# Optimization experiments

Hardware: AMD Instinct MI355X
Metric: run time of the kernel (lower is better)

The kernel has to match this reference:

```python
import jax, jax.numpy as jnp
import numpy as np

V, E, H, L = 100000, 128, 512, 9
B, T = 64, 512


def setup_inputs() -> dict:
    key = jax.random.key(0)
    ks = jax.random.split(key, 8)
    text = jax.random.randint(ks[0], (B, T), 0, V, dtype=jnp.int32)
    labels = jax.random.randint(ks[1], (B, T), 0, L, dtype=jnp.int32)
    embed = jax.random.normal(ks[2], (V, E), jnp.float32) * 0.02
    Wx = jax.random.normal(ks[3], (E, 4 * H), jnp.float32) * (1.0 / np.sqrt(E))
    Wh = jax.random.normal(ks[4], (H, 4 * H), jnp.float32) * (1.0 / np.sqrt(H))
    # Keras LSTM default: zero bias with unit forget-gate bias (gate order i,f,c,o)
    b = jnp.zeros((4 * H,), jnp.float32).at[H:2 * H].set(1.0)
    Wd = jax.random.normal(ks[5], (H, L), jnp.float32) * (1.0 / np.sqrt(H))
    bd = jnp.zeros((L,), jnp.float32)
    trans = jax.random.uniform(ks[6], (L, L), jnp.float32)
    return dict(text=text, labels=labels, embed=embed, Wx=Wx, Wh=Wh, b=b,
                Wd=Wd, bd=bd, trans=trans)


def _lstm(x, Wx, Wh, b):
    # x: [B,T,E] -> h: [B,T,H]; Keras gate order i,f,c,o
    Bx, Tx, _ = x.shape
    Hh = Wh.shape[0]
    xg = jnp.einsum('bte,eg->btg', x, Wx) + b  # precompute input projections [B,T,4H]

    def step(carry, g_t):
        h, c = carry
        g = g_t + h @ Wh
        i, f, cg, o = jnp.split(g, 4, axis=-1)
        c = jax.nn.sigmoid(f) * c + jax.nn.sigmoid(i) * jnp.tanh(cg)
        h = jax.nn.sigmoid(o) * jnp.tanh(c)
        return (h, c), h

    init = (jnp.zeros((Bx, Hh), x.dtype), jnp.zeros((Bx, Hh), x.dtype))
    _, hs = jax.lax.scan(step, init, jnp.moveaxis(xg, 1, 0))
    return jnp.moveaxis(hs, 0, 1)


def _crf_log_likelihood(logits, labels, lens, trans):
    # tfa.text.crf_log_likelihood: score(seq) - log_norm (forward algorithm)
    Bl, Tl, Ll = logits.shape
    t_idx = jnp.arange(Tl)
    mask = t_idx[None, :] < lens[:, None]  # [B,T]
    unary = jnp.take_along_axis(logits, labels[..., None], axis=2)[..., 0]
    unary = jnp.where(mask, unary, 0.0).sum(-1)
    binary = trans[labels[:, :-1], labels[:, 1:]]
    bmask = t_idx[1:][None, :] < lens[:, None]  # transition t->t+1 counts iff t+1 < len
    binary = jnp.where(bmask, binary, 0.0).sum(-1)
    score = unary + binary

    def step(alpha, xs):
        lg, t = xs  # lg: [B,L]
        new = jax.scipy.special.logsumexp(alpha[:, :, None] + trans[None], axis=1) + lg
        alpha = jnp.where((t < lens)[:, None], new, alpha)
        return alpha, None

    alpha0 = logits[:, 0]
    xs = (jnp.moveaxis(logits[:, 1:], 1, 0), jnp.arange(1, Tl))
    alpha, _ = jax.lax.scan(step, alpha0, xs)
    log_norm = jax.scipy.special.logsumexp(alpha, axis=-1)
    return score - log_norm


def reference(text, labels, embed, Wx, Wh, b, Wd, bd, trans):
    lens = jnp.sum((text != 0).astype(jnp.int32), axis=-1)
    x = embed[text]                      # [B,T,E] (dropout inactive at inference)
    h = _lstm(x, Wx, Wh, b)              # [B,T,H]
    logits = h @ Wd + bd                 # [B,T,L]
    ll = _crf_log_likelihood(logits, labels, lens, trans)  # [B]
    return logits, lens, ll
```

## Files before the change

### kernel.cpp

```cpp
#include <hip/hip_runtime.h>
#include <hip/hip_bf16.h>

#define V_SZ 100000
#define E_SZ 128
#define H_SZ 512
#define L_SZ 9
#define B_SZ 64
#define T_SZ 512
#define G4   (4*H_SZ)

#define LOGITS_N (B_SZ*T_SZ*L_SZ)
#define HS_BYTES ((size_t)B_SZ*T_SZ*H_SZ*2)
#define SENT32 0x7FC07FC0u
#define SENT64 0x7FC07FC07FC07FC0ull

typedef short bf16x8 __attribute__((ext_vector_type(8)));
typedef float f32x4  __attribute__((ext_vector_type(4)));

static __device__ __forceinline__ unsigned short f2bf(float x){
  unsigned int u = __builtin_bit_cast(unsigned int, x);
  unsigned int r = (u + 0x7fffu + ((u >> 16) & 1u)) >> 16;
  return (unsigned short)r;
}
static __device__ __forceinline__ float bf2f(unsigned short b){
  unsigned int u = ((unsigned int)b) << 16;
  return __builtin_bit_cast(float, u);
}
static __device__ __forceinline__ float sig_f(float x){
  return 1.f / (1.f + __expf(-x));
}
static __device__ __forceinline__ float tanh_f(float x){
  float a = fabsf(x);
  float e = __expf(-2.f * a);
  float t = (1.f - e) / (1.f + e);
  return copysignf(t, x);
}

__global__ void k_reset(unsigned long long* __restrict__ hs64){
  const long n = HS_BYTES / 8;
  for (long i = (long)blockIdx.x*256 + threadIdx.x; i < n; i += (long)gridDim.x*256)
    __hip_atomic_store(&hs64[i], SENT64, __ATOMIC_RELAXED, __HIP_MEMORY_SCOPE_AGENT);
}

__global__ void k_lens(const int* __restrict__ text, float* __restrict__ out_lens){
  int b = blockIdx.x;
  int c = 0;
  for (int t = threadIdx.x; t < T_SZ; t += 256)
    c += (text[b*T_SZ + t] != 0);
  for (int off = 32; off; off >>= 1) c += __shfl_down(c, off, 64);
  __shared__ int sred[4];
  int w = threadIdx.x >> 6;
  if ((threadIdx.x & 63) == 0) sred[w] = c;
  __syncthreads();
  if (threadIdx.x == 0)
    out_lens[b] = (float)(sred[0] + sred[1] + sred[2] + sred[3]);
}

__global__ __launch_bounds__(256, 1)
void k_lstm(const int* __restrict__ text, const float* __restrict__ embed,
            const float* __restrict__ Wx, const float* __restrict__ Wh,
            const float* __restrict__ bias, unsigned short* __restrict__ hs)
{
  const int g    = blockIdx.x & 7;
  const int j    = blockIdx.x >> 3;
  const int n0   = j * 16;
  const int tid  = threadIdx.x;
  const int w    = tid >> 6;
  const int lane = tid & 63;
  const int q    = lane >> 4;
  const int l16  = lane & 15;
  const int gate = l16 & 3;
  const int cq   = l16 >> 2;

  __shared__ unsigned short h_lds[2][16*512];
  __shared__ unsigned short x_lds[2][16*128];

  for (int i = tid; i < 2*16*512; i += 256) ((unsigned short*)h_lds)[i] = 0;
  for (int i = tid; i < 2*16*128; i += 256) ((unsigned short*)x_lds)[i] = 0;

  const int hcol = n0 + w*4 + cq;
  const int gcol = gate*H_SZ + hcol;
  bf16x8 Whf[16];
#pragma unroll
  for (int kk = 0; kk < 16; ++kk){
    bf16x8 v;
#pragma unroll
    for (int jj = 0; jj < 8; ++jj)
      v[jj] = (short)f2bf(Wh[(long)(kk*32 + q*8 + jj)*G4 + gcol]);
    Whf[kk] = v;
  }
  bf16x8 Wxf[4];
#pragma unroll
  for (int kk = 0; kk < 4; ++kk){
    bf16x8 v;
#pragma unroll
    for (int jj = 0; jj < 8; ++jj)
      v[jj] = (short)f2bf(Wx[(long)(kk*32 + q*8 + jj)*G4 + gcol]);
    Wxf[kk] = v;
  }
  const float biasv = bias[gcol];

  float cs[4] = {0.f, 0.f, 0.f, 0.f};
  const bool isPub = (gate == 0) && ((cq & 1) == 0) && (q < 2);

  unsigned short* ppub[4];
#pragma unroll
  for (int rg = 0; rg < 4; ++rg)
    ppub[rg] = hs + ((long)(g*8 + q*4 + rg)*T_SZ)*H_SZ + n0 + w*4 + cq;

  __syncthreads();

  for (int t = 0; t < T_SZ; ++t){
    const int par = t & 1;

    {
      int xr = tid >> 5;
      int c4 = (tid & 31) * 4;
      int idx = text[(g*8 + xr)*T_SZ + t];
      const float4 xv = *(const float4*)(embed + (long)idx*E_SZ + c4);
      int cb = c4 * 2;
      unsigned short* pp = (unsigned short*)((char*)x_lds[par] + xr*256 + (cb ^ (xr << 4)));
      pp[0] = f2bf(xv.x); pp[1] = f2bf(xv.y); pp[2] = f2bf(xv.z); pp[3] = f2bf(xv.w);
    }

    if (t > 0){
      unsigned long long v[4];
      int it = 0; bool ok;
      do {
        ok = true;
#pragma unroll
        for (int c = 0; c < 4; ++c){
          int chunk = tid + 256*c;
          int hr    = chunk >> 7;
          int k4    = chunk & 127;
          v[c] = __hip_atomic_load(
              (const unsigned long long*)(hs + ((long)(g*8 + hr)*T_SZ + (t-1))*H_SZ + k4*4),
              __ATOMIC_RELAXED, __HIP_MEMORY_SCOPE_AGENT);
        }
#pragma unroll
        for (int c = 0; c < 4; ++c){
          unsigned int lo = (unsigned int)v[c], hi = (unsigned int)(v[c] >> 32);
          ok = ok && (lo != SENT32) && (hi != SENT32);
        }
      } while (!ok && ++it < (1 << 20));
#pragma unroll
      for (int c = 0; c < 4; ++c){
        int chunk = tid + 256*c;
        int hr    = chunk >> 7;
        int k4    = chunk & 127;
        *(unsigned long long*)((char*)h_lds[par] + hr*1024 + ((k4*8) ^ (hr << 4))) = v[c];
      }
    }
    __syncthreads();

    f32x4 acc0 = {biasv, biasv, biasv, biasv};
    f32x4 acc1 = {0.f, 0.f, 0.f, 0.f};
#pragma unroll
    for (int kk = 0; kk < 4; ++kk){
      bf16x8 a = *(const bf16x8*)((const char*)x_lds[par] + l16*256 + ((kk*64 + q*16) ^ (l16 << 4)));
      if (kk & 1) acc1 = __builtin_amdgcn_mfma_f32_16x16x32_bf16(a, Wxf[kk], acc1, 0, 0, 0);
      else        acc0 = __builtin_amdgcn_mfma_f32_16x16x32_bf16(a, Wxf[kk], acc0, 0, 0, 0);
    }
    if (t > 0){
#pragma unroll
      for (int kk = 0; kk < 16; ++kk){
        bf16x8 a = *(const bf16x8*)((const char*)h_lds[par] + l16*1024 + ((kk*64 + q*16) ^ (l16 << 4)));
        if (kk & 1) acc1 = __builtin_amdgcn_mfma_f32_16x16x32_bf16(a, Whf[kk], acc1, 0, 0, 0);
        else        acc0 = __builtin_amdgcn_mfma_f32_16x16x32_bf16(a, Whf[kk], acc0, 0, 0, 0);
      }
    }

#pragma unroll
    for (int rg = 0; rg < 4; ++rg){
      float v  = acc0[rg] + acc1[rg];
      float x1 = __shfl_xor(v, 1, 64);
      float x2 = __shfl_xor(v, 2, 64);
      float x3 = __shfl_xor(v, 3, 64);
      float gi = (gate==0)? v : (gate==1)? x1 : (gate==2)? x2 : x3;
      float gf = (gate==1)? v : (gate==0)? x1 : (gate==3)? x2 : x3;
      float gc = (gate==2)? v : (gate==3)? x1 : (gate==0)? x2 : x3;
      float go = (gate==3)? v : (gate==2)? x1 : (gate==1)? x2 : x3;
      cs[rg] = sig_f(gf)*cs[rg] + sig_f(gi)*tanh_f(gc);
      float hv = sig_f(go)*tanh_f(cs[rg]);
      unsigned int hb = (unsigned int)f2bf(hv);
      unsigned int pr = (unsigned int)__shfl_xor((int)hb, 4, 64);
      unsigned int pk = hb | (pr << 16);
      if (isPub)
        __hip_atomic_store((unsigned int*)ppub[rg], pk,
                           __ATOMIC_RELAXED, __HIP_MEMORY_SCOPE_AGENT);
    }
#pragma unroll
    for (int rg = 0; rg < 4; ++rg) ppub[rg] += H_SZ;
  }
}

__global__ void k_logits(const unsigned short* __restrict__ hs,
                         const float* __restrict__ Wd, const float* __restrict__ bd,
                         float* __restrict__ out)
{
  __shared__ float wd_s[H_SZ*L_SZ];
  __shared__ float bd_s[L_SZ];
  for (int i = threadIdx.x; i < H_SZ*L_SZ; i += 128) wd_s[i] = Wd[i];
  if (threadIdx.x < L_SZ) bd_s[threadIdx.x] = bd[threadIdx.x];
  __syncthreads();

  long row = (long)blockIdx.x*128 + threadIdx.x;
  const unsigned short* hp = hs + row*H_SZ;
  float acc[9];
#pragma unroll
  for (int jj = 0; jj < 9; ++jj) acc[jj] = 0.f;
  for (int k = 0; k < H_SZ; k += 8){
    uint4 v = *(const uint4*)(hp + k);
    const unsigned short* u = (const unsigned short*)&v;
#pragma unroll
    for (int l = 0; l < 8; ++l){
      float hf = bf2f(u[l]);
#pragma unroll
      for (int jj = 0; jj < 9; ++jj)
        acc[jj] = fmaf(hf, wd_s[(k + l)*L_SZ + jj], acc[jj]);
    }
  }
  float* op = out + row*L_SZ;
#pragma unroll
  for (int jj = 0; jj < 9; ++jj) op[jj] = acc[jj] + bd_s[jj];
}

__global__ void k_crf(const float* __restrict__ logits, const int* __restrict__ labels,
                      const float* __restrict__ trans, const float* __restrict__ lensf,
                      float* __restrict__ out_ll)
{
  int b = blockIdx.x;
  int lane = threadIdx.x;
  int len = (int)lensf[b];
  const float* lg  = logits + (long)b*T_SZ*L_SZ;
  const int*   lab = labels + b*T_SZ;

  float s = 0.f;
  for (int t = lane; t < T_SZ; t += 64){
    if (t < len){
      s += lg[t*L_SZ + lab[t]];
      if (t >= 1) s += trans[lab[t-1]*L_SZ + lab[t]];
    }
  }
  for (int off = 32; off; off >>= 1) s += __shfl_down(s, off, 64);

  float tr[9];
#pragma unroll
  for (int i = 0; i < 9; ++i) tr[i] = (lane < 9) ? trans[i*L_SZ + lane] : 0.f;
  float alpha = (lane < 9) ? lg[lane] : -1e30f;

  for (int t = 1; t < T_SZ; ++t){
    float tmp[9];
#pragma unroll
    for (int i = 0; i < 9; ++i){
      float ai = __shfl(alpha, i, 64);
      tmp[i] = ai + tr[i];
    }
    float m0 = fmaxf(fmaxf(tmp[0], tmp[1]), tmp[2]);
    float m1 = fmaxf(fmaxf(tmp[3], tmp[4]), tmp[5]);
    float m2 = fmaxf(fmaxf(tmp[6], tmp[7]), tmp[8]);
    float m  = fmaxf(fmaxf(m0, m1), m2);
    float e = 0.f;
#pragma unroll
    for (int i = 0; i < 9; ++i) e += __expf(tmp[i] - m);
    float lgv = (lane < 9) ? lg[t*L_SZ + lane] : 0.f;
    float nv = m + __logf(e) + lgv;
    if (t < len && lane < 9) alpha = nv;
  }

  float mm = (lane < 9) ? alpha : -1e30f;
  for (int off = 8; off; off >>= 1) mm = fmaxf(mm, __shfl_down(mm, off, 64));
  mm = __shfl(mm, 0, 64);
  float ee = (lane < 9) ? __expf(alpha - mm) : 0.f;
  for (int off = 8; off; off >>= 1) ee += __shfl_down(ee, off, 64);
  if (lane == 0) out_ll[b] = s - (mm + __logf(ee));
}

extern "C" void kernel_launch(void* const* d_in, const int* in_sizes, int n_in,
                              void* d_out, int out_size, void* d_ws, size_t ws_size,
                              hipStream_t stream)
{
  const int*   text   = (const int*)  d_in[0];
  const int*   labels = (const int*)  d_in[1];
  const float* embed  = (const float*)d_in[2];
  const float* Wx     = (const float*)d_in[3];
  const float* Wh     = (const float*)d_in[4];
  const float* bias   = (const float*)d_in[5];
  const float* Wd     = (const float*)d_in[6];
  const float* bd     = (const float*)d_in[7];
  const float* trans  = (const float*)d_in[8];

  float* out        = (float*)d_out;
  float* out_logits = out;
  float* out_lens   = out + LOGITS_N;
  float* out_ll     = out + LOGITS_N + B_SZ;

  unsigned short* hs = (unsigned short*)d_ws;

  k_reset <<<2048, 256, 0, stream>>>((unsigned long long*)hs);
  k_lens  <<<B_SZ, 256, 0, stream>>>(text, out_lens);
  k_lstm  <<<256, 256, 0, stream>>>(text, embed, Wx, Wh, bias, hs);
  k_logits<<<256, 128, 0, stream>>>(hs, Wd, bd, out_logits);
  k_crf   <<<B_SZ, 64, 0, stream>>>(out_logits, labels, trans, out_lens, out_ll);
}
```

Measured before the change: 1.577 ms.

## Prefetch next-step embeddings, cache tokens in LDS, widen h publish stores

Text tokens for the block's rows are staged once into shared memory. The embedding gather for step t+1 is issued after the barrier and written to the other x buffer at the end of step t, so its global latency overlaps the MFMA work instead of sitting on the serial recurrence path. The h publish path now packs four bf16 values into one 64-bit atomic store from a quarter of the lanes instead of 32-bit stores from half. This adds LDS usage and relies on the double-buffered x_lds and the sentinel-polling consumer tolerating 64-bit stores.

```diff
diff --git a/kernel.cpp b/kernel.cpp
--- a/kernel.cpp
+++ b/kernel.cpp
@@ -74,9 +74,12 @@
 
   __shared__ unsigned short h_lds[2][16*512];
   __shared__ unsigned short x_lds[2][16*128];
+  __shared__ int text_lds[8*T_SZ];
 
   for (int i = tid; i < 2*16*512; i += 256) ((unsigned short*)h_lds)[i] = 0;
   for (int i = tid; i < 2*16*128; i += 256) ((unsigned short*)x_lds)[i] = 0;
+  for (int i = tid; i < 8*T_SZ;   i += 256)
+    text_lds[i] = text[(g*8 + (i >> 9))*T_SZ + (i & 511)];
 
   const int hcol = n0 + w*4 + cq;
   const int gcol = gate*H_SZ + hcol;
@@ -101,27 +104,32 @@
   const float biasv = bias[gcol];
 
   float cs[4] = {0.f, 0.f, 0.f, 0.f};
-  const bool isPub = (gate == 0) && ((cq & 1) == 0) && (q < 2);
+  const bool isPub = (gate == 0) && (cq == 0) && (q < 2);
 
   unsigned short* ppub[4];
 #pragma unroll
   for (int rg = 0; rg < 4; ++rg)
-    ppub[rg] = hs + ((long)(g*8 + q*4 + rg)*T_SZ)*H_SZ + n0 + w*4 + cq;
+    ppub[rg] = hs + ((long)(g*8 + q*4 + rg)*T_SZ)*H_SZ + n0 + w*4;
+
+  const int xr = tid >> 5;
+  const int c4 = (tid & 31) * 4;
+  const int cb = c4 * 2;
+  unsigned short* xdst[2];
+#pragma unroll
+  for (int pb = 0; pb < 2; ++pb)
+    xdst[pb] = (unsigned short*)((char*)x_lds[pb] + xr*256 + (cb ^ (xr << 4)));
 
   __syncthreads();
+
+  {
+    int tok = text_lds[xr*T_SZ + 0];
+    const float4 xv = *(const float4*)(embed + (long)tok*E_SZ + c4);
+    unsigned short* pp = xdst[0];
+    pp[0] = f2bf(xv.x); pp[1] = f2bf(xv.y); pp[2] = f2bf(xv.z); pp[3] = f2bf(xv.w);
+  }
 
   for (int t = 0; t < T_SZ; ++t){
     const int par = t & 1;
-
-    {
-      int xr = tid >> 5;
-      int c4 = (tid & 31) * 4;
-      int idx = text[(g*8 + xr)*T_SZ + t];
-      const float4 xv = *(const float4*)(embed + (long)idx*E_SZ + c4);
-      int cb = c4 * 2;
-      unsigned short* pp = (unsigned short*)((char*)x_lds[par] + xr*256 + (cb ^ (xr << 4)));
-      pp[0] = f2bf(xv.x); pp[1] = f2bf(xv.y); pp[2] = f2bf(xv.z); pp[3] = f2bf(xv.w);
-    }
 
     if (t > 0){
       unsigned long long v[4];
@@ -152,6 +160,12 @@
       }
     }
     __syncthreads();
+
+    float4 xv; bool havex = (t + 1 < T_SZ);
+    if (havex){
+      int tok = text_lds[xr*T_SZ + t + 1];
+      xv = *(const float4*)(embed + (long)tok*E_SZ + c4);
+    }
 
     f32x4 acc0 = {biasv, biasv, biasv, biasv};
     f32x4 acc1 = {0.f, 0.f, 0.f, 0.f};
@@ -183,14 +197,22 @@
       cs[rg] = sig_f(gf)*cs[rg] + sig_f(gi)*tanh_f(gc);
       float hv = sig_f(go)*tanh_f(cs[rg]);
       unsigned int hb = (unsigned int)f2bf(hv);
-      unsigned int pr = (unsigned int)__shfl_xor((int)hb, 4, 64);
-      unsigned int pk = hb | (pr << 16);
+      unsigned int pr  = (unsigned int)__shfl_xor((int)hb, 4, 64);
+      unsigned int pk  = hb | (pr << 16);
+      unsigned int pk2 = (unsigned int)__shfl_xor((int)pk, 8, 64);
+      unsigned long long p8 = (unsigned long long)pk
+                            | ((unsigned long long)pk2 << 32);
       if (isPub)
-        __hip_atomic_store((unsigned int*)ppub[rg], pk,
+        __hip_atomic_store((unsigned long long*)ppub[rg], p8,
                            __ATOMIC_RELAXED, __HIP_MEMORY_SCOPE_AGENT);
     }
 #pragma unroll
     for (int rg = 0; rg < 4; ++rg) ppub[rg] += H_SZ;
+
+    if (havex){
+      unsigned short* pp = xdst[par ^ 1];
+      pp[0] = f2bf(xv.x); pp[1] = f2bf(xv.y); pp[2] = f2bf(xv.z); pp[3] = f2bf(xv.w);
+    }
   }
 }
 
```

After: 1.551 ms. About the same (-1.7%).
